# Kernel optimization log

Measured on AMD Instinct MI355X. Metric: run time of the kernel, lower is better.

The kernel has to match this reference:

```python
import jax, jax.numpy as jnp
import numpy as np

N_NODES = 100000
N_EDGES = 800000
IN_FEATS = 128
NUM_CLASSES = 64


def setup_inputs() -> dict:
    key = jax.random.key(0)
    k1, k2, k3, k4 = jax.random.split(key, 4)
    x = jax.random.normal(k1, (N_NODES, IN_FEATS), dtype=jnp.float32)
    edge_src = jax.random.randint(k2, (N_EDGES,), 0, N_NODES, dtype=jnp.int64)
    edge_dst = jax.random.randint(k3, (N_EDGES,), 0, N_NODES, dtype=jnp.int64)
    W_neigh = jax.random.normal(k4, (NUM_CLASSES, IN_FEATS), dtype=jnp.float32) * (1.0 / np.sqrt(IN_FEATS))
    b_neigh = jnp.zeros((NUM_CLASSES,), dtype=jnp.float32)
    return {"x": x, "edge_src": edge_src, "edge_dst": edge_dst,
            "W_neigh": W_neigh, "b_neigh": b_neigh}


def reference(x, edge_src, edge_dst, W_neigh, b_neigh):
    # DGL SAGEConv with aggregator_type='gcn':
    #   h_neigh[v] = (sum_{u->v} x[u] + x[v]) / (in_degree(v) + 1)
    #   out = h_neigh @ W_neigh^T + b_neigh
    n = x.shape[0]
    # gather source features per edge, scatter-sum into destinations
    neigh_sum = jax.ops.segment_sum(x[edge_src], edge_dst, num_segments=n)  # [N, F]
    deg = jax.ops.segment_sum(jnp.ones((edge_src.shape[0],), dtype=x.dtype),
                              edge_dst, num_segments=n)                     # [N]
    h = (neigh_sum + x) / (deg + 1.0)[:, None]
    out = jnp.einsum('nf,cf->nc', h, W_neigh) + b_neigh
    return out
```

## Files before the change

kernel.cpp:

```cpp
#include <hip/hip_runtime.h>

#define N_NODES 100000
#define N_EDGES 800000
#define IN_FEATS 128
#define NUM_CLASSES 64

#define NSB    98
#define SCAP   9216
#define BINCAP 56
#define ECAP   2432

#define K1_GRID 1955

typedef short bf16x8 __attribute__((ext_vector_type(8)));
typedef float f32x4  __attribute__((ext_vector_type(4)));

static __device__ __forceinline__ unsigned short f2bf(float f) {
    unsigned u = __float_as_uint(f);
    unsigned r = (u + 0x7fffu + ((u >> 16) & 1u)) >> 16;
    return (unsigned short)r;
}
static __device__ __forceinline__ float bf2f(unsigned short v) {
    return __uint_as_float(((unsigned)v) << 16);
}

static __device__ __forceinline__ void gemm_body(char* smem, int gid,
                                                 const float* __restrict__ x,
                                                 const float* __restrict__ W,
                                                 unsigned short* __restrict__ y16) {
    const long base = (long)gid * 64;
    if (base >= N_NODES) return;

    unsigned short* Wf = (unsigned short*)smem;
    typedef unsigned short XsRow[136];
    XsRow* Xs = (XsRow*)(smem + 16384);

    const int tid = threadIdx.x;

    for (int i = tid; i < 4 * 4 * 64 * 8; i += 256) {
        const int j    = i & 7;
        const int lane = (i >> 3) & 63;
        const int t    = (i >> 9) & 3;
        const int s    = i >> 11;
        const int k = s * 32 + ((lane >> 4) << 3) + j;
        const int c = t * 16 + (lane & 15);
        Wf[i] = f2bf(W[c * IN_FEATS + k]);
    }

#pragma unroll
    for (int it = 0; it < 8; ++it) {
        const int i   = tid + it * 256;
        const int row = i >> 5;
        const int c4  = (i & 31) << 2;
        const long node = base + row;
        float4 v = make_float4(0.f, 0.f, 0.f, 0.f);
        if (node < N_NODES) v = *(const float4*)&x[node * IN_FEATS + c4];
        ushort4 w4;
        w4.x = f2bf(v.x); w4.y = f2bf(v.y); w4.z = f2bf(v.z); w4.w = f2bf(v.w);
        *(ushort4*)&Xs[row][c4] = w4;
    }
    __syncthreads();

    const int wave = tid >> 6;
    const int lane = tid & 63;
    const long nb  = base + wave * 16;

    bf16x8 wf[4][4];
#pragma unroll
    for (int s = 0; s < 4; ++s)
#pragma unroll
        for (int t = 0; t < 4; ++t)
            wf[s][t] = *(const bf16x8*)&Wf[(((s * 4 + t) * 64) + lane) * 8];

    f32x4 acc[4];
#pragma unroll
    for (int t = 0; t < 4; ++t) acc[t] = (f32x4){0.f, 0.f, 0.f, 0.f};

    const int m  = lane & 15;
    const int kq = lane >> 4;
    const unsigned short* arow = &Xs[wave * 16 + m][kq * 8];

#pragma unroll
    for (int s = 0; s < 4; ++s) {
        bf16x8 af = *(const bf16x8*)(arow + s * 32);
#pragma unroll
        for (int t = 0; t < 4; ++t)
            acc[t] = __builtin_amdgcn_mfma_f32_16x16x32_bf16(af, wf[s][t], acc[t], 0, 0, 0);
    }

    const int ccol  = lane & 15;
    const int rbase = (lane >> 4) << 2;
#pragma unroll
    for (int t = 0; t < 4; ++t)
#pragma unroll
        for (int r = 0; r < 4; ++r)
            Xs[wave * 16 + rbase + r][t * 16 + ccol] = f2bf(acc[t][r]);

    const int orow = lane >> 2;
    const int ocb  = (lane & 3) << 4;
    const long n2  = nb + orow;
    if (n2 < N_NODES) {
        const bf16x8 o0 = *(const bf16x8*)&Xs[wave * 16 + orow][ocb];
        const bf16x8 o1 = *(const bf16x8*)&Xs[wave * 16 + orow][ocb + 8];
        *(bf16x8*)&y16[n2 * NUM_CLASSES + ocb]     = o0;
        *(bf16x8*)&y16[n2 * NUM_CLASSES + ocb + 8] = o1;
    }
}

static __device__ __forceinline__ void p1_body(char* smem, int p1id,
                                               const int* __restrict__ esrc,
                                               const int* __restrict__ edst,
                                               int* __restrict__ sbcur,
                                               unsigned* __restrict__ stage) {
    typedef unsigned BinRow[BINCAP];
    BinRow* bins = (BinRow*)smem;
    int* bcnt  = (int*)(smem + 21952);
    int* bbase = (int*)(smem + 21952 + 392);

    const int tid = threadIdx.x;
    for (int i = tid; i < NSB; i += 256) bcnt[i] = 0;
    __syncthreads();

    const int e0 = p1id * 2048;
#pragma unroll
    for (int it = 0; it < 8; ++it) {
        const int e = e0 + it * 256 + tid;
        if (e < N_EDGES) {
            const unsigned s  = (unsigned)esrc[e];
            const unsigned d  = (unsigned)edst[e];
            const unsigned sb = d >> 10;
            const unsigned pk = s | ((d & 1023u) << 17);
            const int p = atomicAdd(&bcnt[sb], 1);
            if (p < BINCAP) {
                bins[sb][p] = pk;
            } else {
                const int gp = atomicAdd(&sbcur[sb << 4], 1);
                if (gp < SCAP) stage[sb * SCAP + gp] = pk;
            }
        }
    }
    __syncthreads();

    if (tid < NSB) {
        const int c = min(bcnt[tid], BINCAP);
        bcnt[tid]  = c;
        bbase[tid] = atomicAdd(&sbcur[tid << 4], c);
    }
    __syncthreads();

    for (int i = tid; i < NSB * BINCAP; i += 256) {
        const int sb = i / BINCAP;
        const int k  = i - sb * BINCAP;
        if (k < bcnt[sb]) {
            const int pos = bbase[sb] + k;
            if (pos < SCAP) stage[sb * SCAP + pos] = bins[sb][k];
        }
    }
}

__global__ __launch_bounds__(256) void k1_gemm_scatter(const float* __restrict__ x,
                                                       const float* __restrict__ W,
                                                       unsigned short* __restrict__ y16,
                                                       const int* __restrict__ esrc,
                                                       const int* __restrict__ edst,
                                                       int* __restrict__ sbcur,
                                                       unsigned* __restrict__ stage) {
    __shared__ __align__(16) char smem[33792];
    const int bid = blockIdx.x;
    const int r   = bid % 5;
    if (r == 4) {
        p1_body(smem, bid / 5, esrc, edst, sbcur, stage);
    } else {
        gemm_body(smem, (bid / 5) * 4 + r, x, W, y16);
    }
}

__global__ __launch_bounds__(512) void bin_gather(const unsigned* __restrict__ stage,
                                                  const int* __restrict__ sbcur,
                                                  const unsigned short* __restrict__ y16,
                                                  const float* __restrict__ b,
                                                  float* __restrict__ out) {
    __shared__ int lcnt[256];
    __shared__ int loff[256];
    __shared__ int lcur[256];
    __shared__ unsigned entries[ECAP + 8];

    const int sb   = blockIdx.x >> 2;
    const int q    = blockIdx.x & 3;
    const int tid  = threadIdx.x;
    const int wave = tid >> 6;
    const int lane = tid & 63;

    if (tid < 256) lcnt[tid] = 0;
    __syncthreads();

    const int ecnt = min(sbcur[sb << 4], SCAP);
    const unsigned* sp = stage + (size_t)sb * SCAP;

    for (int i = tid; i < ecnt; i += 512) {
        const unsigned dlow = sp[i] >> 17;
        if ((int)(dlow >> 8) == q)
            atomicAdd(&lcnt[dlow & 255u], 1);
    }
    __syncthreads();

    if (tid < 64) {
        const int i0 = tid << 2;
        const int c0 = lcnt[i0], c1 = lcnt[i0 + 1], c2 = lcnt[i0 + 2], c3 = lcnt[i0 + 3];
        const int sum = c0 + c1 + c2 + c3;
        int incl = sum;
#pragma unroll
        for (int s = 1; s < 64; s <<= 1) {
            const int v = __shfl_up(incl, s);
            if (tid >= s) incl += v;
        }
        int run = incl - sum;
        loff[i0]     = min(run, ECAP); lcur[i0]     = min(run, ECAP); run += c0;
        loff[i0 + 1] = min(run, ECAP); lcur[i0 + 1] = min(run, ECAP); run += c1;
        loff[i0 + 2] = min(run, ECAP); lcur[i0 + 2] = min(run, ECAP); run += c2;
        loff[i0 + 3] = min(run, ECAP); lcur[i0 + 3] = min(run, ECAP);
    }
    __syncthreads();

    for (int i = tid; i < ecnt; i += 512) {
        const unsigned pk   = sp[i];
        const unsigned dlow = pk >> 17;
        if ((int)(dlow >> 8) == q) {
            const int pos = atomicAdd(&lcur[dlow & 255u], 1);
            if (pos < ECAP) entries[pos] = pk & 0x1FFFFu;
        }
    }
    __syncthreads();

    const int g     = lane >> 3;
    const int q8    = lane & 7;
    const int gbase = (sb << 10) + (q << 8);

    for (int p = 0; p < 4; ++p) {
        const int ln   = (p << 6) + (wave << 3) + g;
        const int deg  = lcnt[ln];
        const int st   = loff[ln];
        const int degr = min(deg, ECAP - st);

        int mc = degr;
        mc = max(mc, __shfl_xor(mc, 8));
        mc = max(mc, __shfl_xor(mc, 16));
        mc = max(mc, __shfl_xor(mc, 32));
        const int maxd = __builtin_amdgcn_readfirstlane(mc);

        f32x4 accA = {0.f, 0.f, 0.f, 0.f};
        f32x4 accB = {0.f, 0.f, 0.f, 0.f};

        for (int j = 0; j < maxd; j += 8) {
            bf16x8 h[8];
            int    ok[8];
#pragma unroll
            for (int t = 0; t < 8; ++t) {
                const int jt  = j + t;
                ok[t] = (jt < degr);
                const int idx = st + (ok[t] ? jt : 0);
                const unsigned src = entries[idx];
                h[t] = *(const bf16x8*)&y16[(size_t)src * NUM_CLASSES + q8 * 8];
            }
#pragma unroll
            for (int t = 0; t < 8; ++t) {
                if (ok[t]) {
#pragma unroll
                    for (int k = 0; k < 4; ++k) accA[k] += bf2f((unsigned short)h[t][k]);
#pragma unroll
                    for (int k = 0; k < 4; ++k) accB[k] += bf2f((unsigned short)h[t][4 + k]);
                }
            }
        }

        const int gn = gbase + ln;
        if (gn < N_NODES) {
            const bf16x8 hs = *(const bf16x8*)&y16[(size_t)gn * NUM_CLASSES + q8 * 8];
            const float inv = 1.0f / (float)(deg + 1);
            const float4 b0 = *(const float4*)&b[q8 * 8];
            const float4 b1 = *(const float4*)&b[q8 * 8 + 4];

            float4 o0, o1;
            o0.x = (accA[0] + bf2f((unsigned short)hs[0])) * inv + b0.x;
            o0.y = (accA[1] + bf2f((unsigned short)hs[1])) * inv + b0.y;
            o0.z = (accA[2] + bf2f((unsigned short)hs[2])) * inv + b0.z;
            o0.w = (accA[3] + bf2f((unsigned short)hs[3])) * inv + b0.w;
            o1.x = (accB[0] + bf2f((unsigned short)hs[4])) * inv + b1.x;
            o1.y = (accB[1] + bf2f((unsigned short)hs[5])) * inv + b1.y;
            o1.z = (accB[2] + bf2f((unsigned short)hs[6])) * inv + b1.z;
            o1.w = (accB[3] + bf2f((unsigned short)hs[7])) * inv + b1.w;

            *(float4*)&out[(size_t)gn * NUM_CLASSES + q8 * 8]     = o0;
            *(float4*)&out[(size_t)gn * NUM_CLASSES + q8 * 8 + 4] = o1;
        }
    }
}

extern "C" void kernel_launch(void* const* d_in, const int* in_sizes, int n_in,
                              void* d_out, int out_size, void* d_ws, size_t ws_size,
                              hipStream_t stream) {
    const float* x    = (const float*)d_in[0];
    const int*   esrc = (const int*)d_in[1];
    const int*   edst = (const int*)d_in[2];
    const float* W    = (const float*)d_in[3];
    const float* b    = (const float*)d_in[4];
    float* out = (float*)d_out;

    char* p = (char*)d_ws;
    unsigned short* y16 = (unsigned short*)p;  p += (size_t)N_NODES * NUM_CLASSES * 2;
    unsigned* stage     = (unsigned*)p;        p += (size_t)NSB * SCAP * 4;
    int* sbcur          = (int*)p;             p += (size_t)NSB * 16 * 4;

    hipMemsetAsync(sbcur, 0, (size_t)NSB * 16 * 4, stream);

    k1_gemm_scatter<<<K1_GRID, 256, 0, stream>>>(x, W, y16, esrc, edst, sbcur, stage);

    bin_gather<<<NSB * 4, 512, 0, stream>>>(stage, sbcur, y16, b, out);
}
```

Baseline: 144.1 us.

## Rebalance fused GEMM/scatter grid and split gather into eight sub-blocks per superbin

Each GEMM block now processes four 64-node chunks while keeping W fragments in registers, so the fused first kernel drops to a smaller grid with interleaved runs of GEMM and edge-binning blocks. The gather kernel splits each superbin into eight 128-node slices instead of four 256-node slices, which doubles block count and shrinks per-block shared-memory staging. The goal is less redundant W conversion and more parallelism in the gather. The cost is that each gather block rescans the full superbin edge list, and with twice as many blocks that staging read is repeated more often overall.

Result: slower. 156.2 us (+8.4%).

```diff
diff --git a/kernel.cpp b/kernel.cpp
--- a/kernel.cpp
+++ b/kernel.cpp
@@ -8,9 +8,9 @@
 #define NSB    98
 #define SCAP   9216
 #define BINCAP 56
-#define ECAP   2432
-
-#define K1_GRID 1955
+#define ECAP8  1280
+
+#define K1_GRID 784
 
 typedef short bf16x8 __attribute__((ext_vector_type(8)));
 typedef float f32x4  __attribute__((ext_vector_type(4)));
@@ -28,82 +28,90 @@
                                                  const float* __restrict__ x,
                                                  const float* __restrict__ W,
                                                  unsigned short* __restrict__ y16) {
-    const long base = (long)gid * 64;
-    if (base >= N_NODES) return;
+    const long base0 = (long)gid * 256;
+    if (base0 >= N_NODES) return;
 
     unsigned short* Wf = (unsigned short*)smem;
     typedef unsigned short XsRow[136];
     XsRow* Xs = (XsRow*)(smem + 16384);
 
-    const int tid = threadIdx.x;
+    const int tid  = threadIdx.x;
+    const int wave = tid >> 6;
+    const int lane = tid & 63;
 
     for (int i = tid; i < 4 * 4 * 64 * 8; i += 256) {
         const int j    = i & 7;
-        const int lane = (i >> 3) & 63;
+        const int ln   = (i >> 3) & 63;
         const int t    = (i >> 9) & 3;
         const int s    = i >> 11;
-        const int k = s * 32 + ((lane >> 4) << 3) + j;
-        const int c = t * 16 + (lane & 15);
+        const int k = s * 32 + ((ln >> 4) << 3) + j;
+        const int c = t * 16 + (ln & 15);
         Wf[i] = f2bf(W[c * IN_FEATS + k]);
     }
 
-#pragma unroll
-    for (int it = 0; it < 8; ++it) {
-        const int i   = tid + it * 256;
-        const int row = i >> 5;
-        const int c4  = (i & 31) << 2;
-        const long node = base + row;
-        float4 v = make_float4(0.f, 0.f, 0.f, 0.f);
-        if (node < N_NODES) v = *(const float4*)&x[node * IN_FEATS + c4];
-        ushort4 w4;
-        w4.x = f2bf(v.x); w4.y = f2bf(v.y); w4.z = f2bf(v.z); w4.w = f2bf(v.w);
-        *(ushort4*)&Xs[row][c4] = w4;
-    }
-    __syncthreads();
-
-    const int wave = tid >> 6;
-    const int lane = tid & 63;
-    const long nb  = base + wave * 16;
-
     bf16x8 wf[4][4];
-#pragma unroll
-    for (int s = 0; s < 4; ++s)
+
+    for (int ch = 0; ch < 4; ++ch) {
+        const long base = base0 + ch * 64;
+        if (base >= N_NODES) break;
+
+#pragma unroll
+        for (int it = 0; it < 8; ++it) {
+            const int i   = tid + it * 256;
+            const int row = i >> 5;
+            const int c4  = (i & 31) << 2;
+            const long node = base + row;
+            float4 v = make_float4(0.f, 0.f, 0.f, 0.f);
+            if (node < N_NODES) v = *(const float4*)&x[node * IN_FEATS + c4];
+            ushort4 w4;
+            w4.x = f2bf(v.x); w4.y = f2bf(v.y); w4.z = f2bf(v.z); w4.w = f2bf(v.w);
+            *(ushort4*)&Xs[row][c4] = w4;
+        }
+        __syncthreads();
+
+        if (ch == 0) {
+#pragma unroll
+            for (int s = 0; s < 4; ++s)
+#pragma unroll
+                for (int t = 0; t < 4; ++t)
+                    wf[s][t] = *(const bf16x8*)&Wf[(((s * 4 + t) * 64) + lane) * 8];
+        }
+
+        f32x4 acc[4];
+#pragma unroll
+        for (int t = 0; t < 4; ++t) acc[t] = (f32x4){0.f, 0.f, 0.f, 0.f};
+
+        const int m  = lane & 15;
+        const int kq = lane >> 4;
+        const unsigned short* arow = &Xs[wave * 16 + m][kq * 8];
+
+#pragma unroll
+        for (int s = 0; s < 4; ++s) {
+            bf16x8 af = *(const bf16x8*)(arow + s * 32);
+#pragma unroll
+            for (int t = 0; t < 4; ++t)
+                acc[t] = __builtin_amdgcn_mfma_f32_16x16x32_bf16(af, wf[s][t], acc[t], 0, 0, 0);
+        }
+
+        const int ccol  = lane & 15;
+        const int rbase = (lane >> 4) << 2;
 #pragma unroll
         for (int t = 0; t < 4; ++t)
-            wf[s][t] = *(const bf16x8*)&Wf[(((s * 4 + t) * 64) + lane) * 8];
-
-    f32x4 acc[4];
-#pragma unroll
-    for (int t = 0; t < 4; ++t) acc[t] = (f32x4){0.f, 0.f, 0.f, 0.f};
-
-    const int m  = lane & 15;
-    const int kq = lane >> 4;
-    const unsigned short* arow = &Xs[wave * 16 + m][kq * 8];
-
-#pragma unroll
-    for (int s = 0; s < 4; ++s) {
-        bf16x8 af = *(const bf16x8*)(arow + s * 32);
-#pragma unroll
-        for (int t = 0; t < 4; ++t)
-            acc[t] = __builtin_amdgcn_mfma_f32_16x16x32_bf16(af, wf[s][t], acc[t], 0, 0, 0);
-    }
-
-    const int ccol  = lane & 15;
-    const int rbase = (lane >> 4) << 2;
-#pragma unroll
-    for (int t = 0; t < 4; ++t)
-#pragma unroll
-        for (int r = 0; r < 4; ++r)
-            Xs[wave * 16 + rbase + r][t * 16 + ccol] = f2bf(acc[t][r]);
-
-    const int orow = lane >> 2;
-    const int ocb  = (lane & 3) << 4;
-    const long n2  = nb + orow;
-    if (n2 < N_NODES) {
-        const bf16x8 o0 = *(const bf16x8*)&Xs[wave * 16 + orow][ocb];
-        const bf16x8 o1 = *(const bf16x8*)&Xs[wave * 16 + orow][ocb + 8];
-        *(bf16x8*)&y16[n2 * NUM_CLASSES + ocb]     = o0;
-        *(bf16x8*)&y16[n2 * NUM_CLASSES + ocb + 8] = o1;
+#pragma unroll
+            for (int r = 0; r < 4; ++r)
+                Xs[wave * 16 + rbase + r][t * 16 + ccol] = f2bf(acc[t][r]);
+
+        const long nb   = base + wave * 16;
+        const int  orow = lane >> 2;
+        const int  ocb  = (lane & 3) << 4;
+        const long n2   = nb + orow;
+        if (n2 < N_NODES) {
+            const bf16x8 o0 = *(const bf16x8*)&Xs[wave * 16 + orow][ocb];
+            const bf16x8 o1 = *(const bf16x8*)&Xs[wave * 16 + orow][ocb + 8];
+            *(bf16x8*)&y16[n2 * NUM_CLASSES + ocb]     = o0;
+            *(bf16x8*)&y16[n2 * NUM_CLASSES + ocb + 8] = o1;
+        }
+        __syncthreads();
     }
 }
 
@@ -167,11 +175,12 @@
                                                        unsigned* __restrict__ stage) {
     __shared__ __align__(16) char smem[33792];
     const int bid = blockIdx.x;
-    const int r   = bid % 5;
-    if (r == 4) {
-        p1_body(smem, bid / 5, esrc, edst, sbcur, stage);
+    const int run = bid >> 3;
+    const int idx = ((run >> 1) << 3) | (bid & 7);
+    if (run & 1) {
+        p1_body(smem, idx, esrc, edst, sbcur, stage);
     } else {
-        gemm_body(smem, (bid / 5) * 4 + r, x, W, y16);
+        gemm_body(smem, idx, x, W, y16);
     }
 }
 
@@ -180,18 +189,18 @@
                                                   const unsigned short* __restrict__ y16,
                                                   const float* __restrict__ b,
                                                   float* __restrict__ out) {
-    __shared__ int lcnt[256];
-    __shared__ int loff[256];
-    __shared__ int lcur[256];
-    __shared__ unsigned entries[ECAP + 8];
-
-    const int sb   = blockIdx.x >> 2;
-    const int q    = blockIdx.x & 3;
+    __shared__ int lcnt[128];
+    __shared__ int loff[128];
+    __shared__ int lcur[128];
+    __shared__ unsigned entries[ECAP8 + 8];
+
+    const int sb   = blockIdx.x >> 3;
+    const int o    = blockIdx.x & 7;
     const int tid  = threadIdx.x;
     const int wave = tid >> 6;
     const int lane = tid & 63;
 
-    if (tid < 256) lcnt[tid] = 0;
+    if (tid < 128) lcnt[tid] = 0;
     __syncthreads();
 
     const int ecnt = min(sbcur[sb << 4], SCAP);
@@ -199,15 +208,15 @@
 
     for (int i = tid; i < ecnt; i += 512) {
         const unsigned dlow = sp[i] >> 17;
-        if ((int)(dlow >> 8) == q)
-            atomicAdd(&lcnt[dlow & 255u], 1);
+        if ((int)(dlow >> 7) == o)
+            atomicAdd(&lcnt[dlow & 127u], 1);
     }
     __syncthreads();
 
     if (tid < 64) {
-        const int i0 = tid << 2;
-        const int c0 = lcnt[i0], c1 = lcnt[i0 + 1], c2 = lcnt[i0 + 2], c3 = lcnt[i0 + 3];
-        const int sum = c0 + c1 + c2 + c3;
+        const int i0 = tid << 1;
+        const int c0 = lcnt[i0], c1 = lcnt[i0 + 1];
+        const int sum = c0 + c1;
         int incl = sum;
 #pragma unroll
         for (int s = 1; s < 64; s <<= 1) {
@@ -215,32 +224,31 @@
             if (tid >= s) incl += v;
         }
         int run = incl - sum;
-        loff[i0]     = min(run, ECAP); lcur[i0]     = min(run, ECAP); run += c0;
-        loff[i0 + 1] = min(run, ECAP); lcur[i0 + 1] = min(run, ECAP); run += c1;
-        loff[i0 + 2] = min(run, ECAP); lcur[i0 + 2] = min(run, ECAP); run += c2;
-        loff[i0 + 3] = min(run, ECAP); lcur[i0 + 3] = min(run, ECAP);
+        loff[i0]     = min(run, ECAP8); lcur[i0]     = min(run, ECAP8); run += c0;
+        loff[i0 + 1] = min(run, ECAP8); lcur[i0 + 1] = min(run, ECAP8);
     }
     __syncthreads();
 
     for (int i = tid; i < ecnt; i += 512) {
         const unsigned pk   = sp[i];
         const unsigned dlow = pk >> 17;
-        if ((int)(dlow >> 8) == q) {
-            const int pos = atomicAdd(&lcur[dlow & 255u], 1);
-            if (pos < ECAP) entries[pos] = pk & 0x1FFFFu;
+        if ((int)(dlow >> 7) == o) {
+            const int pos = atomicAdd(&lcur[dlow & 127u], 1);
+            if (pos < ECAP8) entries[pos] = pk & 0x1FFFFu;
         }
     }
     __syncthreads();
 
     const int g     = lane >> 3;
     const int q8    = lane & 7;
-    const int gbase = (sb << 10) + (q << 8);
-
-    for (int p = 0; p < 4; ++p) {
+    const int gbase = (sb << 10) + (o << 7);
+
+#pragma unroll
+    for (int p = 0; p < 2; ++p) {
         const int ln   = (p << 6) + (wave << 3) + g;
         const int deg  = lcnt[ln];
         const int st   = loff[ln];
-        const int degr = min(deg, ECAP - st);
+        const int degr = min(deg, ECAP8 - st);
 
         int mc = degr;
         mc = max(mc, __shfl_xor(mc, 8));
@@ -315,5 +323,5 @@
 
     k1_gemm_scatter<<<K1_GRID, 256, 0, stream>>>(x, W, y16, esrc, edst, sbcur, stage);
 
-    bin_gather<<<NSB * 4, 512, 0, stream>>>(stage, sbcur, y16, b, out);
-}
+    bin_gather<<<NSB * 8, 512, 0, stream>>>(stage, sbcur, y16, b, out);
+}
```
